# Performance work log

Hardware: AMD Instinct MI355X
Metric: run time of the kernel (lower is better)

Reference implementation:

```python
import jax, jax.numpy as jnp
import numpy as np
from functools import partial

IMG = 800.0
LEVEL_HW = [13, 25, 50, 100, 200]  # p6..p2 (reverse-sorted dict order)
NUM_A = 3
A_TOTAL = NUM_A * sum(h * h for h in LEVEL_HW)  # 159882


def _rand_boxes(key, shape, img=IMG):
    k1, k2, k3, k4 = jax.random.split(key, 4)
    cx = jax.random.uniform(k1, shape, minval=0.0, maxval=img)
    cy = jax.random.uniform(k2, shape, minval=0.0, maxval=img)
    w = jax.random.uniform(k3, shape, minval=16.0, maxval=256.0)
    h = jax.random.uniform(k4, shape, minval=16.0, maxval=256.0)
    return jnp.stack([cx - w / 2, cy - h / 2, cx + w / 2, cy + h / 2], axis=-1)


def setup_inputs() -> dict:
    key = jax.random.key(0)
    ks = jax.random.split(key, 16)
    feats = {}
    for i, (name, hw) in enumerate(zip(['f_p6', 'f_p5', 'f_p4', 'f_p3', 'f_p2'], LEVEL_HW)):
        feats[name] = jax.random.normal(ks[i], (2, 256, hw, hw), dtype=jnp.float32)
    anchors = _rand_boxes(ks[5], (A_TOTAL,))
    gt_bboxes = _rand_boxes(ks[6], (2, 20))
    w_in = jax.random.normal(ks[7], (256, 256, 3, 3), dtype=jnp.float32) * 0.02
    b_in = jnp.zeros((256,), jnp.float32)
    w_obj = jax.random.normal(ks[8], (3, 256, 1, 1), dtype=jnp.float32) * 0.02
    b_obj = jnp.zeros((3,), jnp.float32)
    w_del = jax.random.normal(ks[9], (12, 256, 1, 1), dtype=jnp.float32) * 0.02
    b_del = jnp.zeros((12,), jnp.float32)
    return dict(**feats, anchors=anchors, gt_bboxes=gt_bboxes,
                w_in=w_in, b_in=b_in, w_obj=w_obj, b_obj=b_obj,
                w_del=w_del, b_del=b_del)


def _conv(x, w, b, pad):
    y = jax.lax.conv_general_dilated(x, w, (1, 1), [(pad, pad), (pad, pad)],
                                     dimension_numbers=('NCHW', 'OIHW', 'NCHW'))
    return y + b[None, :, None, None]


def _pairwise_iou(b1, b2):
    # b1 [A,4], b2 [G,4] -> [A,G]
    a1 = (b1[:, 2] - b1[:, 0]) * (b1[:, 3] - b1[:, 1])
    a2 = (b2[:, 2] - b2[:, 0]) * (b2[:, 3] - b2[:, 1])
    lt = jnp.maximum(b1[:, None, :2], b2[None, :, :2])
    rb = jnp.minimum(b1[:, None, 2:], b2[None, :, 2:])
    wh = jnp.clip(rb - lt, 0.0)
    inter = wh[..., 0] * wh[..., 1]
    return inter / (a1[:, None] + a2[None, :] - inter)


def _get_deltas(src, tgt):
    sw = src[:, 2] - src[:, 0]; sh = src[:, 3] - src[:, 1]
    scx = src[:, 0] + 0.5 * sw; scy = src[:, 1] + 0.5 * sh
    tw = tgt[:, 2] - tgt[:, 0]; th = tgt[:, 3] - tgt[:, 1]
    tcx = tgt[:, 0] + 0.5 * tw; tcy = tgt[:, 1] + 0.5 * th
    return jnp.stack([(tcx - scx) / sw, (tcy - scy) / sh,
                      jnp.log(tw / sw), jnp.log(th / sh)], axis=-1)


def _per_image(logits, deltas, gt, anchors):
    # logits [A], deltas [A,4], gt [G,4]
    iou = _pairwise_iou(anchors, gt)                      # [A,G]
    matched = jnp.argmax(iou, axis=1)                     # [A]
    mval = jnp.max(iou, axis=1)
    label = jnp.where(mval >= 0.7, 1.0, jnp.where(mval < 0.3, 0.0, -1.0))
    # low-quality matches: best anchor per gt is positive
    best_per_gt = jnp.max(iou, axis=0)                    # [G]
    lq = jnp.any((iou == best_per_gt[None, :]) & (best_per_gt[None, :] > 0), axis=1)
    label = jnp.where(lq, 1.0, label)
    # deterministic subsample: up to 128 pos, fill to 256 with neg
    pos_mask = label == 1.0
    neg_mask = label == 0.0
    sel_pos = pos_mask & (jnp.cumsum(pos_mask.astype(jnp.int32)) <= 128)
    n_pos = jnp.sum(sel_pos.astype(jnp.int32))
    sel_neg = neg_mask & (jnp.cumsum(neg_mask.astype(jnp.int32)) <= (256 - n_pos))
    valid = sel_pos | sel_neg
    # BCE with logits, sum over sampled anchors
    tgt = jnp.clip(label, 0.0, 1.0)
    bce = jnp.maximum(logits, 0.0) - logits * tgt + jnp.log1p(jnp.exp(-jnp.abs(logits)))
    obj_loss = jnp.sum(jnp.where(valid, bce, 0.0))
    # smooth-L1 with beta=0 == L1, only on positives
    gt_d = _get_deltas(anchors, gt[matched])              # [A,4]
    l1 = jnp.sum(jnp.abs(deltas - gt_d), axis=-1)
    loc_loss = jnp.sum(jnp.where(sel_pos, l1, 0.0))
    return obj_loss, loc_loss


def _forward(f_p6, f_p5, f_p4, f_p3, f_p2, anchors, gt_bboxes,
             w_in, b_in, w_obj, b_obj, w_del, b_del):
    logits_all, deltas_all = [], []
    for fm in (f_p6, f_p5, f_p4, f_p3, f_p2):  # reverse-sorted fm order
        x = jax.nn.relu(_conv(fm, w_in, b_in, 1))
        lg = _conv(x, w_obj, b_obj, 0)                    # [B,3,H,W]
        dl = _conv(x, w_del, b_del, 0)                    # [B,12,H,W]
        B, _, H, W = lg.shape
        logits_all.append(jnp.transpose(lg, (0, 2, 3, 1)).reshape(B, -1))
        dl = dl.reshape(B, NUM_A, 4, H, W)
        deltas_all.append(jnp.transpose(dl, (0, 3, 4, 1, 2)).reshape(B, -1, 4))
    logits = jnp.concatenate(logits_all, axis=1)          # [B,A]
    deltas = jnp.concatenate(deltas_all, axis=1)          # [B,A,4]
    obj, loc = jax.vmap(_per_image, in_axes=(0, 0, 0, None))(logits, deltas, gt_bboxes, anchors)
    return (obj[0] + obj[1]) / 2.0, (loc[0] + loc[1]) / 2.0


def reference(f_p6, f_p5, f_p4, f_p3, f_p2, anchors, gt_bboxes,
              w_in, b_in, w_obj, b_obj, w_del, b_del):
    return _forward(f_p6, f_p5, f_p4, f_p3, f_p2, anchors, gt_bboxes,
                    w_in, b_in, w_obj, b_obj, w_del, b_del)
```

## Files before the change

### kernel.cpp

```cpp
#include <hip/hip_runtime.h>
#include <hip/hip_bf16.h>
#include <math.h>

#define A_TOTAL 159882
#define NGT 20
#define NBLK 625
#define WTBLK 288


__device__ __forceinline__ float iou_one(float ax1, float ay1, float ax2, float ay2,
                                         float gx1, float gy1, float gx2, float gy2) {
    float a1 = (ax2 - ax1) * (ay2 - ay1);
    float a2 = (gx2 - gx1) * (gy2 - gy1);
    float ltx = fmaxf(ax1, gx1), lty = fmaxf(ay1, gy1);
    float rbx = fminf(ax2, gx2), rby = fminf(ay2, gy2);
    float w = fmaxf(rbx - ltx, 0.f), h = fmaxf(rby - lty, 0.f);
    float inter = w * h;
    return inter / (a1 + a2 - inter);
}

__device__ __forceinline__ void decode_anchor(int a, int& W, int& aid, int& y, int& x, int& lvl) {
    int off;
    if      (a < 507)   { off = 0;     W = 13;  lvl = 0; }
    else if (a < 2382)  { off = 507;   W = 25;  lvl = 1; }
    else if (a < 9882)  { off = 2382;  W = 50;  lvl = 2; }
    else if (a < 39882) { off = 9882;  W = 100; lvl = 3; }
    else                { off = 39882; W = 200; lvl = 4; }
    int rel = a - off;
    aid = rel % 3;
    int pos = rel / 3;
    y = pos / W; x = pos % W;
}

__global__ __launch_bounds__(256) void k1_bmax_wtrans(
    const float* __restrict__ anchors, const float* __restrict__ gt,
    const float* __restrict__ w_in,
    float* __restrict__ pmax, float* __restrict__ mv, unsigned* __restrict__ aux,
    float* __restrict__ wt) {
    const int bx = blockIdx.x, img = blockIdx.y;
    const int tid = threadIdx.x;
    if (bx >= NBLK) {
        int idx = ((bx - NBLK) * 2 + img) * 256 + tid;
        int co = idx / 576, k4 = idx - co * 576;
        float4 v = *(const float4*)(w_in + (size_t)co * 2304 + k4 * 4);
        ((float4*)wt)[(size_t)k4 * 256 + co] = v;
        return;
    }
    __shared__ float sgt[NGT * 4];
    __shared__ float sred[4][NGT];
    __shared__ float pblk[NGT];
    if (tid < NGT * 4) sgt[tid] = gt[img * NGT * 4 + tid];
    __syncthreads();
    const int a = bx * 256 + tid;
    const bool act = a < A_TOTAL;
    float4 ab = make_float4(0.f, 0.f, 1.f, 1.f);
    if (act) ab = ((const float4*)anchors)[a];
    const int lane = tid & 63, wid = tid >> 6;
    float v[NGT];
    float mval = -1.f; int arg = 0;
    #pragma unroll
    for (int g = 0; g < NGT; g++) {
        float u = act ? iou_one(ab.x, ab.y, ab.z, ab.w,
                                sgt[g*4], sgt[g*4+1], sgt[g*4+2], sgt[g*4+3]) : 0.f;
        v[g] = u;
        if (u > mval) { mval = u; arg = g; }
    }
    #pragma unroll
    for (int g = 0; g < NGT; g++) {
        float u = v[g];
        #pragma unroll
        for (int o = 32; o > 0; o >>= 1) u = fmaxf(u, __shfl_down(u, o));
        if (lane == 0) sred[wid][g] = u;
    }
    __syncthreads();
    if (tid < NGT) {
        float u = fmaxf(fmaxf(sred[0][tid], sred[1][tid]),
                        fmaxf(sred[2][tid], sred[3][tid]));
        pblk[tid] = u;
        pmax[((size_t)img * NBLK + bx) * NGT + tid] = u;
    }
    __syncthreads();
    if (act) {
        unsigned mask = 0;
        #pragma unroll
        for (int g = 0; g < NGT; g++)
            if (v[g] == pblk[g] && v[g] > 0.f) mask |= (1u << g);
        mv[(size_t)img * A_TOTAL + a] = mval;
        aux[(size_t)img * A_TOTAL + a] = (mask << 5) | (unsigned)arg;
    }
}

__global__ void k_bred(const float* __restrict__ pmax, unsigned int* __restrict__ best) {
    const int g = blockIdx.x, img = blockIdx.y;
    const int tid = threadIdx.x;
    float v = 0.f;
    for (int i = tid; i < NBLK; i += 256)
        v = fmaxf(v, pmax[((size_t)img * NBLK + i) * NGT + g]);
    const int lane = tid & 63, wid = tid >> 6;
    #pragma unroll
    for (int o = 32; o > 0; o >>= 1) v = fmaxf(v, __shfl_down(v, o));
    __shared__ float r[4];
    if (lane == 0) r[wid] = v;
    __syncthreads();
    if (tid == 0)
        best[img * NGT + g] = __float_as_uint(fmaxf(fmaxf(r[0], r[1]), fmaxf(r[2], r[3])));
}

__global__ __launch_bounds__(256) void k2_label(
    const float* __restrict__ mv, const unsigned* __restrict__ aux,
    const float* __restrict__ pmax, const unsigned int* __restrict__ best,
    unsigned char* __restrict__ packed, unsigned int* __restrict__ blk_cnt) {
    const int img = blockIdx.y, blk = blockIdx.x;
    const int tid = threadIdx.x;
    const int lane = tid & 63, wid = tid >> 6;
    __shared__ float sbest[NGT], pblk[NGT];
    __shared__ int wp[4], wn[4];
    if (tid < NGT) {
        sbest[tid] = __uint_as_float(best[img * NGT + tid]);
        pblk[tid]  = pmax[((size_t)img * NBLK + blk) * NGT + tid];
    }
    __syncthreads();
    const int a = blk * 256 + tid;
    const bool act = a < A_TOTAL;
    int code = 2;
    if (act) {
        float mval = mv[(size_t)img * A_TOTAL + a];
        unsigned ax = aux[(size_t)img * A_TOTAL + a];
        unsigned mask = ax >> 5;
        bool lq = false;
        #pragma unroll
        for (int g = 0; g < NGT; g++)
            if (((mask >> g) & 1u) && (pblk[g] == sbest[g])) lq = true;
        if (lq || mval >= 0.7f) code = 1;
        else if (mval < 0.3f)   code = 0;
        packed[(size_t)img * A_TOTAL + a] = (unsigned char)((code << 5) | (ax & 31u));
    }
    unsigned long long bp = __ballot(act && code == 1);
    unsigned long long bn = __ballot(act && code == 0);
    if (lane == 0) { wp[wid] = __popcll(bp); wn[wid] = __popcll(bn); }
    __syncthreads();
    if (tid == 0) {
        unsigned int p = wp[0] + wp[1] + wp[2] + wp[3];
        unsigned int n = wn[0] + wn[1] + wn[2] + wn[3];
        blk_cnt[img * NBLK + blk] = (p << 16) | n;
    }
}

__global__ __launch_bounds__(256) void k3_select(
    const unsigned char* __restrict__ packed,
    const unsigned int* __restrict__ blk_cnt,
    int* __restrict__ sel, int* __restrict__ sel_count) {
    const int img = blockIdx.y, blk = blockIdx.x;
    const int tid = threadIdx.x;
    const int lane = tid & 63, wid = tid >> 6;
    __shared__ unsigned long long sscan[8];
    __shared__ int wcnt[8];

    unsigned long long tot = 0ULL, pre = 0ULL;
    const int j0 = tid * 3;
    #pragma unroll
    for (int j = 0; j < 3; j++) {
        int i = j0 + j;
        if (i < NBLK) {
            unsigned u = blk_cnt[img * NBLK + i];
            unsigned long long w = ((unsigned long long)(u >> 16) << 32) | (u & 0xFFFFu);
            tot += w;
            if (i < blk) pre += w;
        }
    }
    #pragma unroll
    for (int o = 32; o > 0; o >>= 1) {
        tot += __shfl_down(tot, o);
        pre += __shfl_down(pre, o);
    }
    if (lane == 0) { sscan[wid] = tot; sscan[4 + wid] = pre; }
    __syncthreads();
    unsigned long long tota = sscan[0] + sscan[1] + sscan[2] + sscan[3];
    unsigned long long prea = sscan[4] + sscan[5] + sscan[6] + sscan[7];
    int tp = (int)(tota >> 32), tn = (int)(tota & 0xFFFFFFFFull);
    int npos = min(tp, 128), capn = 256 - npos;
    if (blk == 0 && tid == 0) sel_count[img] = npos + min(tn, capn);
    int base_p = (int)(prea >> 32), base_n = (int)(prea & 0xFFFFFFFFull);

    const int a = blk * 256 + tid;
    const bool act = a < A_TOTAL;
    int code = act ? (packed[(size_t)img * A_TOTAL + a] >> 5) : 2;
    const bool isp = act && code == 1;
    const bool isn = act && code == 0;
    unsigned long long bp = __ballot(isp);
    unsigned long long bn = __ballot(isn);
    if (lane == 0) { wcnt[wid] = __popcll(bp); wcnt[4 + wid] = __popcll(bn); }
    __syncthreads();
    const unsigned long long mlt = (1ULL << lane) - 1ULL;
    int rp = __popcll(bp & mlt), rn = __popcll(bn & mlt);
    for (int w = 0; w < 4; w++)
        if (w < wid) { rp += wcnt[w]; rn += wcnt[4 + w]; }
    if (isp) { int r = base_p + rp; if (r < npos) sel[img * 256 + r] = a | (1 << 30); }
    if (isn) { int r = base_n + rn; if (r < capn) sel[img * 256 + npos + r] = a; }
}

__global__ __launch_bounds__(256) void k_convT16(
    const float* __restrict__ f0, const float* __restrict__ f1,
    const float* __restrict__ f2, const float* __restrict__ f3,
    const float* __restrict__ f4,
    const float* __restrict__ wt,
    const int* __restrict__ sel, const int* __restrict__ sel_count,
    float* __restrict__ xpart) {
    const int img = blockIdx.z;
    const int chunk = blockIdx.y;
    const int slot0 = blockIdx.x * 8;
    const int nsel = sel_count[img];
    if (slot0 >= nsel) return;

    __shared__ __align__(16) float patch[8][144];
    __shared__ int sW[8], sY[8], sX[8], sAct[8];
    __shared__ const float* sfm[8];
    const int tid = threadIdx.x;

    if (tid < 8) {
        int slot = slot0 + tid;
        bool act = slot < nsel;
        int e = act ? sel[img * 256 + slot] : 0;
        int a = e & 0x3FFFFFFF;
        int W, aid, y, x, lvl;
        decode_anchor(a, W, aid, y, x, lvl);
        sW[tid] = W; sY[tid] = y; sX[tid] = x; sAct[tid] = act ? 1 : 0;
        sfm[tid] = (lvl == 0 ? f0 : lvl == 1 ? f1 : lvl == 2 ? f2 : lvl == 3 ? f3 : f4);
    }
    __syncthreads();

    for (int p = tid; p < 8 * 144; p += 256) {
        int aa = p / 144;
        int idx = p - aa * 144;
        int cil = idx / 9;
        int r = idx - cil * 9;
        int ky = r / 3, kx = r - ky * 3;
        int W = sW[aa];
        int yy = sY[aa] + ky - 1, xx = sX[aa] + kx - 1;
        float v = 0.f;
        if (sAct[aa] && yy >= 0 && yy < W && xx >= 0 && xx < W) {
            int ci = chunk * 16 + cil;
            v = sfm[aa][(((size_t)img * 256 + ci) * W + yy) * W + xx];
        }
        patch[aa][idx] = v;
    }
    __syncthreads();

    const int c = tid;
    const float4* wt4 = (const float4*)wt + (size_t)(chunk * 36) * 256 + c;
    float acc[8] = {0.f, 0.f, 0.f, 0.f, 0.f, 0.f, 0.f, 0.f};
    #pragma unroll 4
    for (int i = 0; i < 36; i++) {
        float4 w = wt4[(size_t)i * 256];
        #pragma unroll
        for (int aa = 0; aa < 8; aa++) {
            float4 q = ((const float4*)patch[aa])[i];
            acc[aa] += w.x * q.x + w.y * q.y + w.z * q.z + w.w * q.w;
        }
    }
    #pragma unroll
    for (int aa = 0; aa < 8; aa++) {
        int slot = slot0 + aa;
        if (slot < nsel)
            xpart[(((size_t)img * 16 + chunk) * 256 + slot) * 256 + c] = acc[aa];
    }
}

__global__ __launch_bounds__(256) void k_post16(
    const float* __restrict__ xpart,
    const float* __restrict__ anchors, const float* __restrict__ gt,
    const float* __restrict__ b_in,
    const float* __restrict__ w_obj, const float* __restrict__ b_obj,
    const float* __restrict__ w_del, const float* __restrict__ b_del,
    const unsigned char* __restrict__ packed,
    const int* __restrict__ sel, const int* __restrict__ sel_count,
    float* __restrict__ lossbuf) {
    const int img = blockIdx.y;
    const int slot = blockIdx.x;
    const int nsel = sel_count[img];
    if (slot >= nsel) return;
    const int e = sel[img * 256 + slot];
    const int is_pos = (e >> 30) & 1;
    const int a = e & 0x3FFFFFFF;
    int W, aid, y, x, lvl;
    decode_anchor(a, W, aid, y, x, lvl);

    const int c = threadIdx.x;
    float s = b_in[c];
    #pragma unroll
    for (int ch = 0; ch < 16; ch++)
        s += xpart[(((size_t)img * 16 + ch) * 256 + slot) * 256 + c];
    float xf = fmaxf(s, 0.f);

    float part[5];
    part[0] = xf * w_obj[aid * 256 + c];
    #pragma unroll
    for (int j = 0; j < 4; j++) part[1 + j] = xf * w_del[(aid * 4 + j) * 256 + c];
    const int lane = c & 63, wid = c >> 6;
    __shared__ float red[5][4];
    #pragma unroll
    for (int o = 32; o > 0; o >>= 1)
        #pragma unroll
        for (int j = 0; j < 5; j++) part[j] += __shfl_down(part[j], o);
    if (lane == 0)
        #pragma unroll
        for (int j = 0; j < 5; j++) red[j][wid] = part[j];
    __syncthreads();

    if (c == 0) {
        float logit = red[0][0] + red[0][1] + red[0][2] + red[0][3] + b_obj[aid];
        float tgt = is_pos ? 1.f : 0.f;
        float bce = fmaxf(logit, 0.f) - logit * tgt + log1pf(expf(-fabsf(logit)));
        float l1 = 0.f;
        if (is_pos) {
            float d[4];
            #pragma unroll
            for (int j = 0; j < 4; j++)
                d[j] = red[1 + j][0] + red[1 + j][1] + red[1 + j][2] + red[1 + j][3] + b_del[aid * 4 + j];
            int m = packed[(size_t)img * A_TOTAL + a] & 31;
            const float* sp = anchors + (size_t)a * 4;
            const float* t = gt + (size_t)(img * NGT + m) * 4;
            float sw = sp[2] - sp[0], sh = sp[3] - sp[1];
            float scx = sp[0] + 0.5f * sw, scy = sp[1] + 0.5f * sh;
            float tw = t[2] - t[0], th = t[3] - t[1];
            float tcx = t[0] + 0.5f * tw, tcy = t[1] + 0.5f * th;
            float g0 = (tcx - scx) / sw, g1 = (tcy - scy) / sh;
            float g2 = logf(tw / sw),    g3 = logf(th / sh);
            l1 = fabsf(d[0] - g0) + fabsf(d[1] - g1) + fabsf(d[2] - g2) + fabsf(d[3] - g3);
        }
        lossbuf[(img * 256 + slot) * 2 + 0] = bce;
        lossbuf[(img * 256 + slot) * 2 + 1] = l1;
    }
}

__global__ void k_final(const float* __restrict__ lossbuf,
                        const int* __restrict__ sel_count,
                        float* __restrict__ out) {
    const int t = threadIdx.x;
    const int img = t >> 8, slot = t & 255;
    float bce = 0.f, l1 = 0.f;
    if (slot < sel_count[img]) {
        bce = lossbuf[t * 2 + 0];
        l1  = lossbuf[t * 2 + 1];
    }
    const int lane = t & 63, wid = t >> 6;
    #pragma unroll
    for (int o = 32; o > 0; o >>= 1) {
        bce += __shfl_down(bce, o);
        l1  += __shfl_down(l1, o);
    }
    __shared__ float rb[8], rl[8];
    if (lane == 0) { rb[wid] = bce; rl[wid] = l1; }
    __syncthreads();
    if (t == 0) {
        float sb = 0.f, sl = 0.f;
        #pragma unroll
        for (int w = 0; w < 8; w++) { sb += rb[w]; sl += rl[w]; }
        out[0] = 0.5f * sb;
        out[1] = 0.5f * sl;
    }
}

__global__ void k_init(unsigned int* best, float* out) {
    int t = threadIdx.x;
    if (t < 2 * NGT) best[t] = 0u;
    if (t < 2) out[t] = 0.f;
}

__global__ void k_best(const float* __restrict__ anchors, const float* __restrict__ gt,
                       unsigned int* best) {
    const int img = blockIdx.y;
    __shared__ float sgt[NGT * 4];
    __shared__ float sred[4][NGT];
    const int tid = threadIdx.x;
    if (tid < NGT * 4) sgt[tid] = gt[img * NGT * 4 + tid];
    __syncthreads();
    float vmax[NGT];
    #pragma unroll
    for (int g = 0; g < NGT; g++) vmax[g] = 0.f;
    const int stride = gridDim.x * blockDim.x;
    for (int a = blockIdx.x * blockDim.x + tid; a < A_TOTAL; a += stride) {
        float4 ab = ((const float4*)anchors)[a];
        #pragma unroll
        for (int g = 0; g < NGT; g++) {
            float v = iou_one(ab.x, ab.y, ab.z, ab.w,
                              sgt[g * 4], sgt[g * 4 + 1], sgt[g * 4 + 2], sgt[g * 4 + 3]);
            vmax[g] = fmaxf(vmax[g], v);
        }
    }
    const int lane = tid & 63, wid = tid >> 6;
    #pragma unroll
    for (int g = 0; g < NGT; g++) {
        float v = vmax[g];
        #pragma unroll
        for (int o = 32; o > 0; o >>= 1) v = fmaxf(v, __shfl_down(v, o));
        if (lane == 0) sred[wid][g] = v;
    }
    __syncthreads();
    if (tid < NGT) {
        float v = fmaxf(fmaxf(sred[0][tid], sred[1][tid]),
                        fmaxf(sred[2][tid], sred[3][tid]));
        atomicMax(&best[img * NGT + tid], __float_as_uint(v));
    }
}

__global__ void k_label_old(const float* __restrict__ anchors, const float* __restrict__ gt,
                            const unsigned int* __restrict__ best,
                            unsigned char* packed, unsigned int* blk_cnt) {
    const int img = blockIdx.y;
    __shared__ float sgt[NGT * 4];
    __shared__ unsigned int sbest[NGT];
    __shared__ int wp[4], wn[4];
    const int tid = threadIdx.x;
    if (tid < NGT * 4) sgt[tid] = gt[img * NGT * 4 + tid];
    if (tid < NGT) sbest[tid] = best[img * NGT + tid];
    __syncthreads();
    const int a = blockIdx.x * blockDim.x + tid;
    const bool act = a < A_TOTAL;
    int code = 2;
    if (act) {
        float4 ab = ((const float4*)anchors)[a];
        float mval = -1.f; int arg = 0; bool lq = false;
        #pragma unroll
        for (int g = 0; g < NGT; g++) {
            float v = iou_one(ab.x, ab.y, ab.z, ab.w,
                              sgt[g * 4], sgt[g * 4 + 1], sgt[g * 4 + 2], sgt[g * 4 + 3]);
            if (v > mval) { mval = v; arg = g; }
            if (__float_as_uint(v) == sbest[g] && v > 0.f) lq = true;
        }
        if (lq || mval >= 0.7f) code = 1;
        else if (mval < 0.3f)   code = 0;
        packed[(size_t)img * A_TOTAL + a] = (unsigned char)((code << 5) | arg);
    }
    unsigned long long bp = __ballot(act && code == 1);
    unsigned long long bn = __ballot(act && code == 0);
    const int lane = tid & 63, wid = tid >> 6;
    if (lane == 0) { wp[wid] = __popcll(bp); wn[wid] = __popcll(bn); }
    __syncthreads();
    if (tid == 0) {
        unsigned int p = wp[0] + wp[1] + wp[2] + wp[3];
        unsigned int n = wn[0] + wn[1] + wn[2] + wn[3];
        blk_cnt[img * NBLK + blockIdx.x] = (p << 16) | n;
    }
}

__global__ __launch_bounds__(256) void k_eval(
    const float* __restrict__ f0, const float* __restrict__ f1,
    const float* __restrict__ f2, const float* __restrict__ f3,
    const float* __restrict__ f4,
    const float* __restrict__ anchors, const float* __restrict__ gt,
    const float* __restrict__ w_in, const float* __restrict__ b_in,
    const float* __restrict__ w_obj, const float* __restrict__ b_obj,
    const float* __restrict__ w_del, const float* __restrict__ b_del,
    const unsigned char* __restrict__ packed,
    const int* __restrict__ sel, const int* __restrict__ sel_count,
    float* out) {
    const int img = blockIdx.x >> 6;
    const int slot0 = (blockIdx.x & 63) * 4;
    const int nsel = sel_count[img];
    if (slot0 >= nsel) return;

    __shared__ __align__(16) float patch[4][2304];
    __shared__ float red[4][5][4];
    __shared__ float lsum[2];
    const int c = threadIdx.x;
    if (c < 2) lsum[c] = 0.f;

    bool actv[4]; int av[4], aidv[4], isposv[4];
    #pragma unroll
    for (int aa = 0; aa < 4; aa++) {
        int slot = slot0 + aa;
        bool act = slot < nsel;
        actv[aa] = act;
        int e = act ? sel[img * 256 + slot] : 0;
        isposv[aa] = (e >> 30) & 1;
        int a = e & 0x3FFFFFFF;
        av[aa] = a;
        int W, aid, y, x, lvl;
        decode_anchor(a, W, aid, y, x, lvl);
        aidv[aa] = aid;
        const float* fm = lvl == 0 ? f0 : lvl == 1 ? f1 : lvl == 2 ? f2 : lvl == 3 ? f3 : f4;
        const float* ch = fm + ((size_t)img * 256 + c) * W * W;
        #pragma unroll
        for (int ky = 0; ky < 3; ky++)
            #pragma unroll
            for (int kx = 0; kx < 3; kx++) {
                int yy = y + ky - 1, xx = x + kx - 1;
                float v = (act && yy >= 0 && yy < W && xx >= 0 && xx < W) ? ch[yy * W + xx] : 0.f;
                patch[aa][c * 9 + ky * 3 + kx] = v;
            }
    }
    __syncthreads();

    const float bi = b_in[c];
    float acc0 = bi, acc1 = bi, acc2 = bi, acc3 = bi;
    const float4* wr = (const float4*)(w_in + (size_t)c * 2304);
    const float4* p0 = (const float4*)patch[0];
    const float4* p1 = (const float4*)patch[1];
    const float4* p2 = (const float4*)patch[2];
    const float4* p3 = (const float4*)patch[3];
    #pragma unroll 4
    for (int i = 0; i < 576; i++) {
        float4 w = wr[i];
        float4 q;
        q = p0[i]; acc0 += w.x * q.x + w.y * q.y + w.z * q.z + w.w * q.w;
        q = p1[i]; acc1 += w.x * q.x + w.y * q.y + w.z * q.z + w.w * q.w;
        q = p2[i]; acc2 += w.x * q.x + w.y * q.y + w.z * q.z + w.w * q.w;
        q = p3[i]; acc3 += w.x * q.x + w.y * q.y + w.z * q.z + w.w * q.w;
    }
    float xf[4] = { fmaxf(acc0, 0.f), fmaxf(acc1, 0.f), fmaxf(acc2, 0.f), fmaxf(acc3, 0.f) };

    float part[4][5];
    #pragma unroll
    for (int aa = 0; aa < 4; aa++) {
        part[aa][0] = xf[aa] * w_obj[aidv[aa] * 256 + c];
        #pragma unroll
        for (int j = 0; j < 4; j++)
            part[aa][1 + j] = xf[aa] * w_del[(aidv[aa] * 4 + j) * 256 + c];
    }
    const int lane = c & 63, wid = c >> 6;
    #pragma unroll
    for (int o = 32; o > 0; o >>= 1)
        #pragma unroll
        for (int aa = 0; aa < 4; aa++)
            #pragma unroll
            for (int j = 0; j < 5; j++)
                part[aa][j] += __shfl_down(part[aa][j], o);
    if (lane == 0)
        #pragma unroll
        for (int aa = 0; aa < 4; aa++)
            #pragma unroll
            for (int j = 0; j < 5; j++)
                red[aa][j][wid] = part[aa][j];
    __syncthreads();

    if (c < 4 && actv[c]) {
        const int aa = c;
        float logit = red[aa][0][0] + red[aa][0][1] + red[aa][0][2] + red[aa][0][3] + b_obj[aidv[aa]];
        float tgt = isposv[aa] ? 1.f : 0.f;
        float bce = fmaxf(logit, 0.f) - logit * tgt + log1pf(expf(-fabsf(logit)));
        atomicAdd(&lsum[0], bce);
        if (isposv[aa]) {
            float d[4];
            #pragma unroll
            for (int j = 0; j < 4; j++)
                d[j] = red[aa][1 + j][0] + red[aa][1 + j][1] + red[aa][1 + j][2] + red[aa][1 + j][3]
                       + b_del[aidv[aa] * 4 + j];
            int a = av[aa];
            int m = packed[(size_t)img * A_TOTAL + a] & 31;
            const float* s = anchors + (size_t)a * 4;
            const float* t = gt + (size_t)(img * NGT + m) * 4;
            float sw = s[2] - s[0], sh = s[3] - s[1];
            float scx = s[0] + 0.5f * sw, scy = s[1] + 0.5f * sh;
            float tw = t[2] - t[0], th = t[3] - t[1];
            float tcx = t[0] + 0.5f * tw, tcy = t[1] + 0.5f * th;
            float g0 = (tcx - scx) / sw, g1 = (tcy - scy) / sh;
            float g2 = logf(tw / sw),    g3 = logf(th / sh);
            float l1 = fabsf(d[0] - g0) + fabsf(d[1] - g1) + fabsf(d[2] - g2) + fabsf(d[3] - g3);
            atomicAdd(&lsum[1], l1);
        }
    }
    __syncthreads();
    if (c == 0) {
        atomicAdd(&out[0], 0.5f * lsum[0]);
        atomicAdd(&out[1], 0.5f * lsum[1]);
    }
}

extern "C" void kernel_launch(void* const* d_in, const int* in_sizes, int n_in,
                              void* d_out, int out_size, void* d_ws, size_t ws_size,
                              hipStream_t stream) {
    const float* f_p6 = (const float*)d_in[0];
    const float* f_p5 = (const float*)d_in[1];
    const float* f_p4 = (const float*)d_in[2];
    const float* f_p3 = (const float*)d_in[3];
    const float* f_p2 = (const float*)d_in[4];
    const float* anchors = (const float*)d_in[5];
    const float* gt      = (const float*)d_in[6];
    const float* w_in  = (const float*)d_in[7];
    const float* b_in  = (const float*)d_in[8];
    const float* w_obj = (const float*)d_in[9];
    const float* b_obj = (const float*)d_in[10];
    const float* w_del = (const float*)d_in[11];
    const float* b_del = (const float*)d_in[12];
    float* out = (float*)d_out;
    char* ws = (char*)d_ws;

    unsigned int* best    = (unsigned int*)(ws + 0);
    int* sel_count        = (int*)(ws + 168);
    int* sel              = (int*)(ws + 192);
    unsigned int* blk_cnt = (unsigned int*)(ws + 2240);
    unsigned char* packed = (unsigned char*)(ws + 17344);
    float* lossbuf        = (float*)(ws + 337152);
    float* mv             = (float*)(ws + 341248);
    unsigned* aux         = (unsigned*)(ws + 1620352);
    float* pmax           = (float*)(ws + 2899456);
    float* xpart          = (float*)(ws + 2999552);
    float* wt             = (float*)(ws + 11388160);
    const size_t WS_NEED  = 13747456;

    if (ws_size >= WS_NEED) {
        k1_bmax_wtrans<<<dim3(NBLK + WTBLK, 2), 256, 0, stream>>>(anchors, gt, w_in,
                                                                  pmax, mv, aux, wt);
        k_bred<<<dim3(NGT, 2), 256, 0, stream>>>(pmax, best);
        k2_label<<<dim3(NBLK, 2), 256, 0, stream>>>(mv, aux, pmax, best, packed, blk_cnt);
        k3_select<<<dim3(NBLK, 2), 256, 0, stream>>>(packed, blk_cnt, sel, sel_count);
        k_convT16<<<dim3(32, 16, 2), 256, 0, stream>>>(f_p6, f_p5, f_p4, f_p3, f_p2,
                                                       wt, sel, sel_count, xpart);
        k_post16<<<dim3(256, 2), 256, 0, stream>>>(xpart, anchors, gt, b_in,
                                                   w_obj, b_obj, w_del, b_del,
                                                   packed, sel, sel_count, lossbuf);
        k_final<<<1, 512, 0, stream>>>(lossbuf, sel_count, out);
    } else {
        k_init<<<1, 64, 0, stream>>>(best, out);
        k_best<<<dim3(64, 2), 256, 0, stream>>>(anchors, gt, best);
        k_label_old<<<dim3(NBLK, 2), 256, 0, stream>>>(anchors, gt, best, packed, blk_cnt);
        k3_select<<<dim3(NBLK, 2), 256, 0, stream>>>(packed, blk_cnt, sel, sel_count);
        k_eval<<<128, 256, 0, stream>>>(f_p6, f_p5, f_p4, f_p3, f_p2,
                                        anchors, gt, w_in, b_in, w_obj, b_obj,
                                        w_del, b_del, packed, sel, sel_count, out);
    }
}
```

Measured before the change: 63.16 us.

## Fuse reductions into producer kernels via last-block counters and widen conv tiles

The per-GT best-IoU reduction kernel is folded into the first kernel, and the final loss sum is folded into the post kernel. In both cases an atomic counter lets the last finishing block do the reduction, which removes two kernel launches. The conv kernel now processes 16 selected anchors per block instead of 8, so each weight load is reused twice as often, at the cost of more registers and fewer blocks. A memset is added to reset the counters, and the serial tail reduction in the last block adds latency.

```diff
diff --git a/kernel.cpp b/kernel.cpp
--- a/kernel.cpp
+++ b/kernel.cpp
@@ -32,11 +32,12 @@
     y = pos / W; x = pos % W;
 }
 
-__global__ __launch_bounds__(256) void k1_bmax_wtrans(
+__global__ __launch_bounds__(256) void k1_fused(
     const float* __restrict__ anchors, const float* __restrict__ gt,
     const float* __restrict__ w_in,
     float* __restrict__ pmax, float* __restrict__ mv, unsigned* __restrict__ aux,
-    float* __restrict__ wt) {
+    float* __restrict__ wt, unsigned int* __restrict__ best,
+    unsigned* __restrict__ ctr) {
     const int bx = blockIdx.x, img = blockIdx.y;
     const int tid = threadIdx.x;
     if (bx >= NBLK) {
@@ -49,6 +50,7 @@
     __shared__ float sgt[NGT * 4];
     __shared__ float sred[4][NGT];
     __shared__ float pblk[NGT];
+    __shared__ int sdone;
     if (tid < NGT * 4) sgt[tid] = gt[img * NGT * 4 + tid];
     __syncthreads();
     const int a = bx * 256 + tid;
@@ -88,22 +90,30 @@
         mv[(size_t)img * A_TOTAL + a] = mval;
         aux[(size_t)img * A_TOTAL + a] = (mask << 5) | (unsigned)arg;
     }
-}
-
-__global__ void k_bred(const float* __restrict__ pmax, unsigned int* __restrict__ best) {
-    const int g = blockIdx.x, img = blockIdx.y;
-    const int tid = threadIdx.x;
-    float v = 0.f;
-    for (int i = tid; i < NBLK; i += 256)
-        v = fmaxf(v, pmax[((size_t)img * NBLK + i) * NGT + g]);
-    const int lane = tid & 63, wid = tid >> 6;
-    #pragma unroll
-    for (int o = 32; o > 0; o >>= 1) v = fmaxf(v, __shfl_down(v, o));
-    __shared__ float r[4];
-    if (lane == 0) r[wid] = v;
-    __syncthreads();
-    if (tid == 0)
-        best[img * NGT + g] = __float_as_uint(fmaxf(fmaxf(r[0], r[1]), fmaxf(r[2], r[3])));
+    __syncthreads();
+    if (tid == 0) {
+        __threadfence();
+        int d = (atomicAdd(&ctr[img], 1u) == (unsigned)(NBLK - 1));
+        sdone = d;
+        if (d) __threadfence();
+    }
+    __syncthreads();
+    if (sdone) {
+        #pragma unroll 1
+        for (int g = 0; g < NGT; g++) {
+            float u = 0.f;
+            for (int i = tid; i < NBLK; i += 256)
+                u = fmaxf(u, pmax[((size_t)img * NBLK + i) * NGT + g]);
+            #pragma unroll
+            for (int o = 32; o > 0; o >>= 1) u = fmaxf(u, __shfl_down(u, o));
+            if (lane == 0) sred[wid][g] = u;
+        }
+        __syncthreads();
+        if (tid < NGT)
+            best[img * NGT + tid] = __float_as_uint(
+                fmaxf(fmaxf(sred[0][tid], sred[1][tid]),
+                      fmaxf(sred[2][tid], sred[3][tid])));
+    }
 }
 
 __global__ __launch_bounds__(256) void k2_label(
@@ -199,7 +209,7 @@
     if (isn) { int r = base_n + rn; if (r < capn) sel[img * 256 + npos + r] = a; }
 }
 
-__global__ __launch_bounds__(256) void k_convT16(
+__global__ __launch_bounds__(256) void k_convT16A(
     const float* __restrict__ f0, const float* __restrict__ f1,
     const float* __restrict__ f2, const float* __restrict__ f3,
     const float* __restrict__ f4,
@@ -208,16 +218,16 @@
     float* __restrict__ xpart) {
     const int img = blockIdx.z;
     const int chunk = blockIdx.y;
-    const int slot0 = blockIdx.x * 8;
+    const int slot0 = blockIdx.x * 16;
     const int nsel = sel_count[img];
     if (slot0 >= nsel) return;
 
-    __shared__ __align__(16) float patch[8][144];
-    __shared__ int sW[8], sY[8], sX[8], sAct[8];
-    __shared__ const float* sfm[8];
+    __shared__ __align__(16) float patch[16][144];
+    __shared__ int sW[16], sY[16], sX[16], sAct[16];
+    __shared__ const float* sfm[16];
     const int tid = threadIdx.x;
 
-    if (tid < 8) {
+    if (tid < 16) {
         int slot = slot0 + tid;
         bool act = slot < nsel;
         int e = act ? sel[img * 256 + slot] : 0;
@@ -229,7 +239,7 @@
     }
     __syncthreads();
 
-    for (int p = tid; p < 8 * 144; p += 256) {
+    for (int p = tid; p < 16 * 144; p += 256) {
         int aa = p / 144;
         int idx = p - aa * 144;
         int cil = idx / 9;
@@ -248,25 +258,27 @@
 
     const int c = tid;
     const float4* wt4 = (const float4*)wt + (size_t)(chunk * 36) * 256 + c;
-    float acc[8] = {0.f, 0.f, 0.f, 0.f, 0.f, 0.f, 0.f, 0.f};
-    #pragma unroll 4
+    float acc[16];
+    #pragma unroll
+    for (int aa = 0; aa < 16; aa++) acc[aa] = 0.f;
+    #pragma unroll 2
     for (int i = 0; i < 36; i++) {
         float4 w = wt4[(size_t)i * 256];
         #pragma unroll
-        for (int aa = 0; aa < 8; aa++) {
+        for (int aa = 0; aa < 16; aa++) {
             float4 q = ((const float4*)patch[aa])[i];
             acc[aa] += w.x * q.x + w.y * q.y + w.z * q.z + w.w * q.w;
         }
     }
     #pragma unroll
-    for (int aa = 0; aa < 8; aa++) {
+    for (int aa = 0; aa < 16; aa++) {
         int slot = slot0 + aa;
         if (slot < nsel)
             xpart[(((size_t)img * 16 + chunk) * 256 + slot) * 256 + c] = acc[aa];
     }
 }
 
-__global__ __launch_bounds__(256) void k_post16(
+__global__ __launch_bounds__(256) void k_post_final(
     const float* __restrict__ xpart,
     const float* __restrict__ anchors, const float* __restrict__ gt,
     const float* __restrict__ b_in,
@@ -274,90 +286,98 @@
     const float* __restrict__ w_del, const float* __restrict__ b_del,
     const unsigned char* __restrict__ packed,
     const int* __restrict__ sel, const int* __restrict__ sel_count,
-    float* __restrict__ lossbuf) {
+    float* __restrict__ lossbuf, float* __restrict__ out,
+    unsigned* __restrict__ ctr) {
     const int img = blockIdx.y;
     const int slot = blockIdx.x;
     const int nsel = sel_count[img];
-    if (slot >= nsel) return;
-    const int e = sel[img * 256 + slot];
-    const int is_pos = (e >> 30) & 1;
-    const int a = e & 0x3FFFFFFF;
-    int W, aid, y, x, lvl;
-    decode_anchor(a, W, aid, y, x, lvl);
-
     const int c = threadIdx.x;
-    float s = b_in[c];
-    #pragma unroll
-    for (int ch = 0; ch < 16; ch++)
-        s += xpart[(((size_t)img * 16 + ch) * 256 + slot) * 256 + c];
-    float xf = fmaxf(s, 0.f);
-
-    float part[5];
-    part[0] = xf * w_obj[aid * 256 + c];
-    #pragma unroll
-    for (int j = 0; j < 4; j++) part[1 + j] = xf * w_del[(aid * 4 + j) * 256 + c];
     const int lane = c & 63, wid = c >> 6;
     __shared__ float red[5][4];
-    #pragma unroll
-    for (int o = 32; o > 0; o >>= 1)
-        #pragma unroll
-        for (int j = 0; j < 5; j++) part[j] += __shfl_down(part[j], o);
-    if (lane == 0)
-        #pragma unroll
-        for (int j = 0; j < 5; j++) red[j][wid] = part[j];
-    __syncthreads();
-
+    __shared__ int sdone;
+    __shared__ float rb[4], rl[4];
+
+    if (slot < nsel) {
+        const int e = sel[img * 256 + slot];
+        const int is_pos = (e >> 30) & 1;
+        const int a = e & 0x3FFFFFFF;
+        int W, aid, y, x, lvl;
+        decode_anchor(a, W, aid, y, x, lvl);
+
+        float s = b_in[c];
+        #pragma unroll
+        for (int ch = 0; ch < 16; ch++)
+            s += xpart[(((size_t)img * 16 + ch) * 256 + slot) * 256 + c];
+        float xf = fmaxf(s, 0.f);
+
+        float part[5];
+        part[0] = xf * w_obj[aid * 256 + c];
+        #pragma unroll
+        for (int j = 0; j < 4; j++) part[1 + j] = xf * w_del[(aid * 4 + j) * 256 + c];
+        #pragma unroll
+        for (int o = 32; o > 0; o >>= 1)
+            #pragma unroll
+            for (int j = 0; j < 5; j++) part[j] += __shfl_down(part[j], o);
+        if (lane == 0)
+            #pragma unroll
+            for (int j = 0; j < 5; j++) red[j][wid] = part[j];
+        __syncthreads();
+
+        if (c == 0) {
+            float logit = red[0][0] + red[0][1] + red[0][2] + red[0][3] + b_obj[aid];
+            float tgt = is_pos ? 1.f : 0.f;
+            float bce = fmaxf(logit, 0.f) - logit * tgt + log1pf(expf(-fabsf(logit)));
+            float l1 = 0.f;
+            if (is_pos) {
+                float d[4];
+                #pragma unroll
+                for (int j = 0; j < 4; j++)
+                    d[j] = red[1 + j][0] + red[1 + j][1] + red[1 + j][2] + red[1 + j][3]
+                           + b_del[aid * 4 + j];
+                int m = packed[(size_t)img * A_TOTAL + a] & 31;
+                const float* sp = anchors + (size_t)a * 4;
+                const float* t = gt + (size_t)(img * NGT + m) * 4;
+                float sw = sp[2] - sp[0], sh = sp[3] - sp[1];
+                float scx = sp[0] + 0.5f * sw, scy = sp[1] + 0.5f * sh;
+                float tw = t[2] - t[0], th = t[3] - t[1];
+                float tcx = t[0] + 0.5f * tw, tcy = t[1] + 0.5f * th;
+                float g0 = (tcx - scx) / sw, g1 = (tcy - scy) / sh;
+                float g2 = logf(tw / sw),    g3 = logf(th / sh);
+                l1 = fabsf(d[0]-g0) + fabsf(d[1]-g1) + fabsf(d[2]-g2) + fabsf(d[3]-g3);
+            }
+            lossbuf[(img * 256 + slot) * 2 + 0] = bce;
+            lossbuf[(img * 256 + slot) * 2 + 1] = l1;
+        }
+    }
+    __syncthreads();
     if (c == 0) {
-        float logit = red[0][0] + red[0][1] + red[0][2] + red[0][3] + b_obj[aid];
-        float tgt = is_pos ? 1.f : 0.f;
-        float bce = fmaxf(logit, 0.f) - logit * tgt + log1pf(expf(-fabsf(logit)));
-        float l1 = 0.f;
-        if (is_pos) {
-            float d[4];
-            #pragma unroll
-            for (int j = 0; j < 4; j++)
-                d[j] = red[1 + j][0] + red[1 + j][1] + red[1 + j][2] + red[1 + j][3] + b_del[aid * 4 + j];
-            int m = packed[(size_t)img * A_TOTAL + a] & 31;
-            const float* sp = anchors + (size_t)a * 4;
-            const float* t = gt + (size_t)(img * NGT + m) * 4;
-            float sw = sp[2] - sp[0], sh = sp[3] - sp[1];
-            float scx = sp[0] + 0.5f * sw, scy = sp[1] + 0.5f * sh;
-            float tw = t[2] - t[0], th = t[3] - t[1];
-            float tcx = t[0] + 0.5f * tw, tcy = t[1] + 0.5f * th;
-            float g0 = (tcx - scx) / sw, g1 = (tcy - scy) / sh;
-            float g2 = logf(tw / sw),    g3 = logf(th / sh);
-            l1 = fabsf(d[0] - g0) + fabsf(d[1] - g1) + fabsf(d[2] - g2) + fabsf(d[3] - g3);
-        }
-        lossbuf[(img * 256 + slot) * 2 + 0] = bce;
-        lossbuf[(img * 256 + slot) * 2 + 1] = l1;
-    }
-}
-
-__global__ void k_final(const float* __restrict__ lossbuf,
-                        const int* __restrict__ sel_count,
-                        float* __restrict__ out) {
-    const int t = threadIdx.x;
-    const int img = t >> 8, slot = t & 255;
-    float bce = 0.f, l1 = 0.f;
-    if (slot < sel_count[img]) {
-        bce = lossbuf[t * 2 + 0];
-        l1  = lossbuf[t * 2 + 1];
-    }
-    const int lane = t & 63, wid = t >> 6;
-    #pragma unroll
-    for (int o = 32; o > 0; o >>= 1) {
-        bce += __shfl_down(bce, o);
-        l1  += __shfl_down(l1, o);
-    }
-    __shared__ float rb[8], rl[8];
-    if (lane == 0) { rb[wid] = bce; rl[wid] = l1; }
-    __syncthreads();
-    if (t == 0) {
-        float sb = 0.f, sl = 0.f;
-        #pragma unroll
-        for (int w = 0; w < 8; w++) { sb += rb[w]; sl += rl[w]; }
-        out[0] = 0.5f * sb;
-        out[1] = 0.5f * sl;
+        __threadfence();
+        int d = (atomicAdd(ctr, 1u) == 511u);
+        sdone = d;
+        if (d) __threadfence();
+    }
+    __syncthreads();
+    if (sdone) {
+        int n0 = sel_count[0], n1 = sel_count[1];
+        float bce = 0.f, l1 = 0.f;
+        for (int e2 = c; e2 < 512; e2 += 256) {
+            int i2 = e2 >> 8, s2 = e2 & 255;
+            if (s2 < (i2 ? n1 : n0)) {
+                bce += lossbuf[e2 * 2 + 0];
+                l1  += lossbuf[e2 * 2 + 1];
+            }
+        }
+        #pragma unroll
+        for (int o = 32; o > 0; o >>= 1) {
+            bce += __shfl_down(bce, o);
+            l1  += __shfl_down(l1, o);
+        }
+        if (lane == 0) { rb[wid] = bce; rl[wid] = l1; }
+        __syncthreads();
+        if (c == 0) {
+            out[0] = 0.5f * (rb[0] + rb[1] + rb[2] + rb[3]);
+            out[1] = 0.5f * (rl[0] + rl[1] + rl[2] + rl[3]);
+        }
     }
 }
 
@@ -590,6 +610,7 @@
     int* sel_count        = (int*)(ws + 168);
     int* sel              = (int*)(ws + 192);
     unsigned int* blk_cnt = (unsigned int*)(ws + 2240);
+    unsigned* ctrs        = (unsigned*)(ws + 7296);
     unsigned char* packed = (unsigned char*)(ws + 17344);
     float* lossbuf        = (float*)(ws + 337152);
     float* mv             = (float*)(ws + 341248);
@@ -600,17 +621,17 @@
     const size_t WS_NEED  = 13747456;
 
     if (ws_size >= WS_NEED) {
-        k1_bmax_wtrans<<<dim3(NBLK + WTBLK, 2), 256, 0, stream>>>(anchors, gt, w_in,
-                                                                  pmax, mv, aux, wt);
-        k_bred<<<dim3(NGT, 2), 256, 0, stream>>>(pmax, best);
+        hipMemsetAsync(ctrs, 0, 16, stream);
+        k1_fused<<<dim3(NBLK + WTBLK, 2), 256, 0, stream>>>(anchors, gt, w_in,
+                                                            pmax, mv, aux, wt, best, ctrs);
         k2_label<<<dim3(NBLK, 2), 256, 0, stream>>>(mv, aux, pmax, best, packed, blk_cnt);
         k3_select<<<dim3(NBLK, 2), 256, 0, stream>>>(packed, blk_cnt, sel, sel_count);
-        k_convT16<<<dim3(32, 16, 2), 256, 0, stream>>>(f_p6, f_p5, f_p4, f_p3, f_p2,
-                                                       wt, sel, sel_count, xpart);
-        k_post16<<<dim3(256, 2), 256, 0, stream>>>(xpart, anchors, gt, b_in,
-                                                   w_obj, b_obj, w_del, b_del,
-                                                   packed, sel, sel_count, lossbuf);
-        k_final<<<1, 512, 0, stream>>>(lossbuf, sel_count, out);
+        k_convT16A<<<dim3(16, 16, 2), 256, 0, stream>>>(f_p6, f_p5, f_p4, f_p3, f_p2,
+                                                        wt, sel, sel_count, xpart);
+        k_post_final<<<dim3(256, 2), 256, 0, stream>>>(xpart, anchors, gt, b_in,
+                                                       w_obj, b_obj, w_del, b_del,
+                                                       packed, sel, sel_count,
+                                                       lossbuf, out, ctrs + 2);
     } else {
         k_init<<<1, 64, 0, stream>>>(best, out);
         k_best<<<dim3(64, 2), 256, 0, stream>>>(anchors, gt, best);
```

After: 122.2 us. +93.5%, slower.
